# Kernel optimization log

Measured on AMD Instinct MI355X. Metric: run time of the kernel, lower is better.

The kernel has to match this reference:

```python
import jax, jax.numpy as jnp
import numpy as np

B, S, D = 4, 2048, 1024
H, DK, DV = 16, 64, 64


def setup_inputs() -> dict:
    key = jax.random.key(0)
    ks = jax.random.split(key, 12)
    scale = 1.0 / np.sqrt(D)
    queries = jax.random.normal(ks[0], (B, S, D), dtype=jnp.float32)
    keys_ = jax.random.normal(ks[1], (B, S, D), dtype=jnp.float32)
    values = jax.random.normal(ks[2], (B, S, D), dtype=jnp.float32)
    # binary additive mask (1 = masked out), broadcastable over batch and heads
    mask = jax.random.randint(ks[3], (1, 1, S, S), 0, 2).astype(jnp.float32)
    Wq = jax.random.normal(ks[4], (D, H * DK), dtype=jnp.float32) * scale
    bq = jnp.zeros((H * DK,), dtype=jnp.float32)
    Wk = jax.random.normal(ks[5], (D, H * DK), dtype=jnp.float32) * scale
    bk = jnp.zeros((H * DK,), dtype=jnp.float32)
    Wv = jax.random.normal(ks[6], (D, H * DV), dtype=jnp.float32) * scale
    bv = jnp.zeros((H * DV,), dtype=jnp.float32)
    Wo = jax.random.normal(ks[7], (H * DV, D), dtype=jnp.float32) * scale
    bo = jnp.zeros((D,), dtype=jnp.float32)
    return {"queries": queries, "keys": keys_, "values": values, "mask": mask,
            "Wq": Wq, "bq": bq, "Wk": Wk, "bk": bk, "Wv": Wv, "bv": bv,
            "Wo": Wo, "bo": bo}


def reference(queries, keys, values, mask, Wq, bq, Wk, bk, Wv, bv, Wo, bo):
    b = queries.shape[0]
    # projections + split heads: [B, S, H*Dh] -> [B, H, S, Dh]
    q = (queries @ Wq + bq).reshape(b, -1, H, DK).transpose(0, 2, 1, 3)
    k = (keys @ Wk + bk).reshape(b, -1, H, DK).transpose(0, 2, 1, 3)
    v = (values @ Wv + bv).reshape(b, -1, H, DV).transpose(0, 2, 1, 3)
    scores = jnp.einsum("bhqd,bhkd->bhqk", q, k) / jnp.sqrt(jnp.float32(DK))
    scores = scores + mask * (-1e9)
    attn = jax.nn.softmax(scores, axis=-1)
    ctx = jnp.einsum("bhqk,bhkd->bhqd", attn, v)  # [B, H, S, DV]
    ctx = ctx.transpose(0, 2, 1, 3).reshape(b, -1, H * DV)
    return ctx @ Wo + bo
```

## Files before the change

kernel.cpp:

```cpp
#include <hip/hip_runtime.h>
#include <cstdint>
#include <cstddef>

typedef __attribute__((ext_vector_type(8))) short bf16x8;
typedef __attribute__((ext_vector_type(4))) short bf16x4;
typedef __attribute__((ext_vector_type(4))) float f32x4;

__device__ __forceinline__ unsigned short f2bf(float f) {
    union { float f; unsigned int u; } v; v.f = f;
    unsigned int r = v.u + 0x7FFFu + ((v.u >> 16) & 1u);
    return (unsigned short)(r >> 16);
}
__device__ __forceinline__ unsigned int pk2(float a, float b) {
    return (unsigned int)f2bf(a) | ((unsigned int)f2bf(b) << 16);
}
__device__ __forceinline__ unsigned int pkfast(float a, float b) {
    unsigned int ua = __builtin_bit_cast(unsigned int, a) + 0x8000u;
    unsigned int ub = __builtin_bit_cast(unsigned int, b) + 0x8000u;
    return __builtin_amdgcn_perm(ub, ua, 0x07060302u);
}

typedef __attribute__((address_space(1))) void gvoid;
typedef __attribute__((address_space(3))) void svoid;
__device__ __forceinline__ void ld16_lds(const void* g, void* l) {
    __builtin_amdgcn_global_load_lds((gvoid*)g, (svoid*)l, 16, 0, 0);
}

#define LDT 72
#define QSCALE 0.1803368801111204f

__global__ __launch_bounds__(256)
void prep_weights(const float* __restrict__ W0, const float* __restrict__ W1,
                  const float* __restrict__ W2, const float* __restrict__ W3,
                  unsigned short* __restrict__ T0, unsigned short* __restrict__ T1,
                  unsigned short* __restrict__ T2, unsigned short* __restrict__ T3)
{
    __shared__ float t[32][33];
    const int z = blockIdx.z;
    const float* W = (z == 0) ? W0 : (z == 1) ? W1 : (z == 2) ? W2 : W3;
    unsigned short* Wt = (z == 0) ? T0 : (z == 1) ? T1 : (z == 2) ? T2 : T3;
    const int n0 = blockIdx.x * 32, k0 = blockIdx.y * 32;
    const int tx = threadIdx.x & 31, ty = threadIdx.x >> 5;
#pragma unroll
    for (int i = 0; i < 4; i++)
        t[ty + 8 * i][tx] = W[(size_t)(k0 + ty + 8 * i) * 1024 + n0 + tx];
    __syncthreads();
#pragma unroll
    for (int i = 0; i < 4; i++)
        Wt[(size_t)(n0 + ty + 8 * i) * 1024 + k0 + tx] = f2bf(t[tx][ty + 8 * i]);
}

__global__ __launch_bounds__(256)
void mask_pack(const float* __restrict__ m, unsigned long long* __restrict__ bits)
{
    const int wv = (blockIdx.x << 2) | (threadIdx.x >> 6);
    const int lane = threadIdx.x & 63;
    for (int i = 0; i < 64; i++) {
        const size_t word = (size_t)wv * 64 + i;
        const float v = m[word * 64 + lane];
        unsigned long long b = __ballot(v != 0.0f);
        if (lane == 0) bits[word] = b;
    }
}

template <int MODE>
__global__ __launch_bounds__(256, 2)
void gemm128(const float* __restrict__ A32, const unsigned short* __restrict__ A16,
             const unsigned short* __restrict__ Wt, const float* __restrict__ bias,
             unsigned short* __restrict__ ob, float* __restrict__ of)
{
    __shared__ __align__(16) unsigned short sm[2 * 128 * LDT];
    unsigned short* As = sm;
    unsigned short* Bs = sm + 128 * LDT;

    const int tid  = threadIdx.x;
    const int lane = tid & 63;
    const int wave = tid >> 6;
    const int quad = lane >> 4;
    const int l16  = lane & 15;
    const int wr   = wave >> 1;
    const int wc   = wave & 1;

    const int m0 = blockIdx.x * 128;
    const int n0 = blockIdx.y * 128;

    const int sr = tid >> 1;
    const int sh = (tid & 1) << 4;

    f32x4 acc[4][4];
#pragma unroll
    for (int i = 0; i < 4; i++)
#pragma unroll
        for (int j = 0; j < 4; j++) acc[i][j] = (f32x4){0.f, 0.f, 0.f, 0.f};

    for (int kk = 0; kk < 1024; kk += 32) {
        if (MODE < 3) {
            const float* g = A32 + (size_t)(m0 + sr) * 1024 + kk + sh;
            float4 a0 = *(const float4*)(g);
            float4 a1 = *(const float4*)(g + 4);
            float4 a2 = *(const float4*)(g + 8);
            float4 a3 = *(const float4*)(g + 12);
            uint4 p0, p1;
            p0.x = pk2(a0.x, a0.y); p0.y = pk2(a0.z, a0.w);
            p0.z = pk2(a1.x, a1.y); p0.w = pk2(a1.z, a1.w);
            p1.x = pk2(a2.x, a2.y); p1.y = pk2(a2.z, a2.w);
            p1.z = pk2(a3.x, a3.y); p1.w = pk2(a3.z, a3.w);
            *(uint4*)&As[sr * LDT + sh]     = p0;
            *(uint4*)&As[sr * LDT + sh + 8] = p1;
        } else {
            const uint4* g = (const uint4*)(A16 + (size_t)(m0 + sr) * 1024 + kk + sh);
            *(uint4*)&As[sr * LDT + sh]     = g[0];
            *(uint4*)&As[sr * LDT + sh + 8] = g[1];
        }
        {
            const uint4* g = (const uint4*)(Wt + (size_t)(n0 + sr) * 1024 + kk + sh);
            *(uint4*)&Bs[sr * LDT + sh]     = g[0];
            *(uint4*)&Bs[sr * LDT + sh + 8] = g[1];
        }
        __syncthreads();

        bf16x8 af[4], bfr[4];
#pragma unroll
        for (int mt = 0; mt < 4; mt++)
            af[mt] = *(const bf16x8*)&As[(wr * 64 + mt * 16 + l16) * LDT + quad * 8];
#pragma unroll
        for (int nt = 0; nt < 4; nt++)
            bfr[nt] = *(const bf16x8*)&Bs[(wc * 64 + nt * 16 + l16) * LDT + quad * 8];
#pragma unroll
        for (int mt = 0; mt < 4; mt++)
#pragma unroll
            for (int nt = 0; nt < 4; nt++)
                acc[mt][nt] = __builtin_amdgcn_mfma_f32_16x16x32_bf16(af[mt], bfr[nt], acc[mt][nt], 0, 0, 0);
        __syncthreads();
    }

    float bv[4];
#pragma unroll
    for (int nt = 0; nt < 4; nt++) bv[nt] = bias[n0 + wc * 64 + nt * 16 + l16];

    if (MODE == 3) {
#pragma unroll
        for (int mt = 0; mt < 4; mt++) {
            const int m = m0 + wr * 64 + mt * 16 + quad * 4;
#pragma unroll
            for (int nt = 0; nt < 4; nt++) {
                const int n = n0 + wc * 64 + nt * 16 + l16;
#pragma unroll
                for (int r = 0; r < 4; r++)
                    of[(size_t)(m + r) * 1024 + n] = acc[mt][nt][r] + bv[nt];
            }
        }
    } else if (MODE == 0 || MODE == 1) {
#pragma unroll
        for (int mt = 0; mt < 4; mt++) {
            const int m = m0 + wr * 64 + mt * 16 + quad * 4;
            const int b = m >> 11;
#pragma unroll
            for (int nt = 0; nt < 4; nt++) {
                const int n = n0 + wc * 64 + nt * 16 + l16;
                const int h = n >> 6, dk = n & 63;
#pragma unroll
                for (int r = 0; r < 4; r++) {
                    const int s = (m + r) & 2047;
                    float o = acc[mt][nt][r] + bv[nt];
                    if (MODE == 0) o *= QSCALE;
                    ob[((size_t)((b << 4) + h) * 2048 + s) * 64 + dk] = f2bf(o);
                }
            }
        }
    } else {
        unsigned short* T = sm + wave * (64 * LDT);
#pragma unroll
        for (int mt = 0; mt < 4; mt++)
#pragma unroll
            for (int nt = 0; nt < 4; nt++)
#pragma unroll
                for (int r = 0; r < 4; r++)
                    T[(nt * 16 + l16) * LDT + mt * 16 + quad * 4 + r] = f2bf(acc[mt][nt][r] + bv[nt]);
        __syncthreads();
#pragma unroll
        for (int i = 0; i < 8; i++) {
            const int nl = i * 8 + (lane >> 3);
            const int mc = lane & 7;
            uint4 v = *(const uint4*)&T[nl * LDT + mc * 8];
            const int n  = n0 + wc * 64 + nl;
            const int mg = m0 + wr * 64 + mc * 8;
            const int b = mg >> 11, s = mg & 2047;
            const int h = n >> 6, dv = n & 63;
            *(uint4*)&ob[((size_t)((b << 4) + h) * 64 + dv) * 2048 + s] = v;
        }
    }
}

__global__ __launch_bounds__(256, 4)
void attn_kernel(const unsigned short* __restrict__ q,
                 const unsigned short* __restrict__ k,
                 const unsigned short* __restrict__ vT,
                 const unsigned int* __restrict__ mbits,
                 unsigned short* __restrict__ ctx)
{
    __shared__ __align__(16) unsigned short Ks[2][64 * 64];
    __shared__ __align__(16) unsigned short Vs[2][64 * 64];

    const int tid = threadIdx.x, lane = tid & 63, wave = tid >> 6;
    const int quad = lane >> 4, l16 = lane & 15;
    const int sw = l16 & 7;
    const int bid = blockIdx.x;
    const int qblk = bid & 15, h = (bid >> 4) & 15, b = bid >> 8;

    const unsigned short* qb = q  + (size_t)(b * 16 + h) * 2048 * 64;
    const unsigned short* kb = k  + (size_t)(b * 16 + h) * 2048 * 64;
    const unsigned short* vb = vT + (size_t)(b * 16 + h) * 64 * 2048;

    const int c0 = tid, c1 = 256 + tid;
    const int r0 = c0 >> 3, gcc0 = (c0 & 7) ^ (r0 & 7);
    const int r1 = c1 >> 3, gcc1 = (c1 & 7) ^ (r1 & 7);

    int qrow[2];
    bf16x8 qf[2][2];
    f32x4 O0[4], O1[4];
    float l_i[2] = {0.f, 0.f};
#pragma unroll
    for (int g = 0; g < 2; g++) {
        qrow[g] = qblk * 128 + wave * 32 + g * 16 + l16;
        qf[g][0] = *(const bf16x8*)&qb[qrow[g] * 64 + quad * 8];
        qf[g][1] = *(const bf16x8*)&qb[qrow[g] * 64 + 32 + quad * 8];
    }
#pragma unroll
    for (int i = 0; i < 4; i++) { O0[i] = (f32x4){0.f,0.f,0.f,0.f}; O1[i] = (f32x4){0.f,0.f,0.f,0.f}; }
    const unsigned int* mrow0 = mbits + (size_t)qrow[0] * 64;
    const unsigned int* mrow1 = mbits + (size_t)qrow[1] * 64;

    {
        ld16_lds((const char*)kb + (size_t)r0 * 128 + gcc0 * 16, (char*)Ks[0] + c0 * 16);
        ld16_lds((const char*)kb + (size_t)r1 * 128 + gcc1 * 16, (char*)Ks[0] + c1 * 16);
        ld16_lds((const char*)vb + (size_t)r0 * 4096 + gcc0 * 16, (char*)Vs[0] + c0 * 16);
        ld16_lds((const char*)vb + (size_t)r1 * 4096 + gcc1 * 16, (char*)Vs[0] + c1 * 16);
    }
    uint2 mwc0 = *(const uint2*)&mrow0[0];
    uint2 mwc1 = *(const uint2*)&mrow1[0];

    for (int it = 0; it < 32; ++it) {
        const int kt = it << 6;
        const int cur = it & 1, nxt = cur ^ 1;
        __syncthreads();

        if (it < 31) {
            const char* kg = (const char*)kb + (size_t)(kt + 64) * 128;
            const char* vg = (const char*)vb + (size_t)(kt + 64) * 2;
            ld16_lds(kg + (size_t)r0 * 128 + gcc0 * 16, (char*)Ks[nxt] + c0 * 16);
            ld16_lds(kg + (size_t)r1 * 128 + gcc1 * 16, (char*)Ks[nxt] + c1 * 16);
            ld16_lds(vg + (size_t)r0 * 4096 + gcc0 * 16, (char*)Vs[nxt] + c0 * 16);
            ld16_lds(vg + (size_t)r1 * 4096 + gcc1 * 16, (char*)Vs[nxt] + c1 * 16);
        }
        const int mi = (it < 31) ? ((kt + 64) >> 5) : 0;
        uint2 mwn0 = *(const uint2*)&mrow0[mi];
        uint2 mwn1 = *(const uint2*)&mrow1[mi];

        const unsigned short* Kc = Ks[cur];
        const unsigned short* Vc = Vs[cur];

        f32x4 S0[4], S1[4];
#pragma unroll
        for (int mt = 0; mt < 4; mt++) {
            const unsigned short* kp = Kc + (mt * 16 + l16) * 64;
            bf16x8 ka0 = *(const bf16x8*)&kp[((quad    ) ^ sw) * 8];
            bf16x8 ka1 = *(const bf16x8*)&kp[((4 + quad) ^ sw) * 8];
            f32x4 z0 = (f32x4){0.f,0.f,0.f,0.f};
            f32x4 z1 = (f32x4){0.f,0.f,0.f,0.f};
            z0 = __builtin_amdgcn_mfma_f32_16x16x32_bf16(ka0, qf[0][0], z0, 0, 0, 0);
            S0[mt] = __builtin_amdgcn_mfma_f32_16x16x32_bf16(ka1, qf[0][1], z0, 0, 0, 0);
            z1 = __builtin_amdgcn_mfma_f32_16x16x32_bf16(ka0, qf[1][0], z1, 0, 0, 0);
            S1[mt] = __builtin_amdgcn_mfma_f32_16x16x32_bf16(ka1, qf[1][1], z1, 0, 0, 0);
        }
        float sum0 = 0.f, sum1 = 0.f;
        bf16x4 pf0[4], pf1[4];
#pragma unroll
        for (int mt = 0; mt < 4; mt++) {
            const unsigned int wm0 = ((mt & 2) ? mwc0.y : mwc0.x) >> (((mt & 1) << 4) + (quad << 2));
            const unsigned int wm1 = ((mt & 2) ? mwc1.y : mwc1.x) >> (((mt & 1) << 4) + (quad << 2));
#pragma unroll
            for (int r = 0; r < 4; r++) {
                float s0 = ((wm0 >> r) & 1u) ? -1e8f : S0[mt][r];
                float s1 = ((wm1 >> r) & 1u) ? -1e8f : S1[mt][r];
                s0 = __builtin_amdgcn_exp2f(s0);
                s1 = __builtin_amdgcn_exp2f(s1);
                S0[mt][r] = s0; sum0 += s0;
                S1[mt][r] = s1; sum1 += s1;
            }
            uint2 u0, u1;
            u0.x = pkfast(S0[mt][0], S0[mt][1]); u0.y = pkfast(S0[mt][2], S0[mt][3]);
            u1.x = pkfast(S1[mt][0], S1[mt][1]); u1.y = pkfast(S1[mt][2], S1[mt][3]);
            pf0[mt] = __builtin_bit_cast(bf16x4, u0);
            pf1[mt] = __builtin_bit_cast(bf16x4, u1);
        }
        sum0 += __shfl_xor(sum0, 16); sum0 += __shfl_xor(sum0, 32);
        sum1 += __shfl_xor(sum1, 16); sum1 += __shfl_xor(sum1, 32);
        l_i[0] += sum0; l_i[1] += sum1;

#pragma unroll
        for (int dvt = 0; dvt < 4; dvt++) {
            const unsigned short* vp = Vc + (dvt * 16 + l16) * 64;
#pragma unroll
            for (int mt = 0; mt < 4; mt++) {
                uint2 vv = *(const uint2*)&vp[((2 * mt + (quad >> 1)) ^ sw) * 8 + (quad & 1) * 4];
                bf16x4 va = __builtin_bit_cast(bf16x4, vv);
                O0[dvt] = __builtin_amdgcn_mfma_f32_16x16x16bf16_1k(va, pf0[mt], O0[dvt], 0, 0, 0);
                O1[dvt] = __builtin_amdgcn_mfma_f32_16x16x16bf16_1k(va, pf1[mt], O1[dvt], 0, 0, 0);
            }
        }
        mwc0 = mwn0; mwc1 = mwn1;
    }
#pragma unroll
    for (int g = 0; g < 2; g++) {
        const float rl = __builtin_amdgcn_rcpf(l_i[g]);
        const f32x4* O = g ? O1 : O0;
#pragma unroll
        for (int dvt = 0; dvt < 4; dvt++) {
            uint2 st;
            st.x = pk2(O[dvt][0] * rl, O[dvt][1] * rl);
            st.y = pk2(O[dvt][2] * rl, O[dvt][3] * rl);
            *(uint2*)&ctx[(size_t)(b * 2048 + qrow[g]) * 1024 + h * 64 + dvt * 16 + quad * 4] = st;
        }
    }
}

extern "C" void kernel_launch(void* const* d_in, const int* in_sizes, int n_in,
                              void* d_out, int out_size, void* d_ws, size_t ws_size,
                              hipStream_t stream)
{
    const float* Qin = (const float*)d_in[0];
    const float* Kin = (const float*)d_in[1];
    const float* Vin = (const float*)d_in[2];
    const float* Msk = (const float*)d_in[3];
    const float* Wq  = (const float*)d_in[4];
    const float* bq  = (const float*)d_in[5];
    const float* Wk  = (const float*)d_in[6];
    const float* bk  = (const float*)d_in[7];
    const float* Wv  = (const float*)d_in[8];
    const float* bv  = (const float*)d_in[9];
    const float* Wo  = (const float*)d_in[10];
    const float* bo  = (const float*)d_in[11];

    unsigned short* w = (unsigned short*)d_ws;
    unsigned short* wtq  = w;
    unsigned short* wtk  = w + (1u << 20);
    unsigned short* wtv  = w + 2u * (1u << 20);
    unsigned short* wto  = w + 3u * (1u << 20);
    unsigned short* qb   = w + 4u * (1u << 20);
    unsigned short* kb   = qb + (1u << 23);
    unsigned short* vTb  = kb + (1u << 23);
    unsigned short* ctxb = vTb + (1u << 23);
    unsigned long long* mb = (unsigned long long*)(ctxb + (1u << 23));

    prep_weights<<<dim3(32, 32, 4), 256, 0, stream>>>(Wq, Wk, Wv, Wo, wtq, wtk, wtv, wto);
    mask_pack<<<256, 256, 0, stream>>>(Msk, mb);
    gemm128<0><<<dim3(64, 8), 256, 0, stream>>>(Qin, nullptr, wtq, bq, qb, nullptr);
    gemm128<1><<<dim3(64, 8), 256, 0, stream>>>(Kin, nullptr, wtk, bk, kb, nullptr);
    gemm128<2><<<dim3(64, 8), 256, 0, stream>>>(Vin, nullptr, wtv, bv, vTb, nullptr);
    attn_kernel<<<1024, 256, 0, stream>>>(qb, kb, vTb, (const unsigned int*)mb, ctxb);
    gemm128<3><<<dim3(64, 8), 256, 0, stream>>>(nullptr, ctxb, wto, bo, nullptr, (float*)d_out);
}
```

Baseline: 453.1 us.

## Pre-convert inputs to bf16 and stage GEMM tiles via direct global-to-LDS loads

Adds a separate pass that converts the fp32 query, key and value inputs to bf16 once. The projection GEMMs then load bf16 tiles straight into LDS with global_load_lds instead of loading fp32 into registers, converting, and storing. This removes the repeated per-tile conversion and halves the bytes each of the 8 column blocks re-reads, at the cost of an extra full read and write pass over the inputs. The LDS tile padding is also dropped, which risks bank conflicts on fragment reads. Separately, the attention softmax denominator's cross-lane shuffle reduction moves out of the key loop to a single reduction at the end.

```diff
diff --git a/kernel.cpp b/kernel.cpp
--- a/kernel.cpp
+++ b/kernel.cpp
@@ -26,8 +26,24 @@
     __builtin_amdgcn_global_load_lds((gvoid*)g, (svoid*)l, 16, 0, 0);
 }
 
-#define LDT 72
 #define QSCALE 0.1803368801111204f
+
+__global__ __launch_bounds__(256)
+void cvt_bf16(const float* __restrict__ A, const float* __restrict__ B,
+              const float* __restrict__ C,
+              unsigned short* __restrict__ oa, unsigned short* __restrict__ ob,
+              unsigned short* __restrict__ oc)
+{
+    const float* src = (blockIdx.y == 0) ? A : (blockIdx.y == 1) ? B : C;
+    unsigned short* dst = (blockIdx.y == 0) ? oa : (blockIdx.y == 1) ? ob : oc;
+    const size_t i = ((size_t)blockIdx.x * 256 + threadIdx.x) * 8;
+    float4 a = *(const float4*)(src + i);
+    float4 b = *(const float4*)(src + i + 4);
+    uint4 p;
+    p.x = pk2(a.x, a.y); p.y = pk2(a.z, a.w);
+    p.z = pk2(b.x, b.y); p.w = pk2(b.z, b.w);
+    *(uint4*)(dst + i) = p;
+}
 
 __global__ __launch_bounds__(256)
 void prep_weights(const float* __restrict__ W0, const float* __restrict__ W1,
@@ -65,13 +81,13 @@
 
 template <int MODE>
 __global__ __launch_bounds__(256, 2)
-void gemm128(const float* __restrict__ A32, const unsigned short* __restrict__ A16,
+void gemm128(const unsigned short* __restrict__ A,
              const unsigned short* __restrict__ Wt, const float* __restrict__ bias,
              unsigned short* __restrict__ ob, float* __restrict__ of)
 {
-    __shared__ __align__(16) unsigned short sm[2 * 128 * LDT];
+    __shared__ __align__(16) unsigned short sm[(MODE == 2) ? 18432 : 8192];
     unsigned short* As = sm;
-    unsigned short* Bs = sm + 128 * LDT;
+    unsigned short* Bs = sm + 4096;
 
     const int tid  = threadIdx.x;
     const int lane = tid & 63;
@@ -84,8 +100,11 @@
     const int m0 = blockIdx.x * 128;
     const int n0 = blockIdx.y * 128;
 
-    const int sr = tid >> 1;
-    const int sh = (tid & 1) << 4;
+    const int sr0 = tid >> 2,        sc0 = (tid & 3) << 4;
+    const int sr1 = sr0 + 64,        sc1 = sc0;
+
+    const char* Ab = (const char*)A  + (size_t)m0 * 2048;
+    const char* Bb = (const char*)Wt + (size_t)n0 * 2048;
 
     f32x4 acc[4][4];
 #pragma unroll
@@ -94,38 +113,20 @@
         for (int j = 0; j < 4; j++) acc[i][j] = (f32x4){0.f, 0.f, 0.f, 0.f};
 
     for (int kk = 0; kk < 1024; kk += 32) {
-        if (MODE < 3) {
-            const float* g = A32 + (size_t)(m0 + sr) * 1024 + kk + sh;
-            float4 a0 = *(const float4*)(g);
-            float4 a1 = *(const float4*)(g + 4);
-            float4 a2 = *(const float4*)(g + 8);
-            float4 a3 = *(const float4*)(g + 12);
-            uint4 p0, p1;
-            p0.x = pk2(a0.x, a0.y); p0.y = pk2(a0.z, a0.w);
-            p0.z = pk2(a1.x, a1.y); p0.w = pk2(a1.z, a1.w);
-            p1.x = pk2(a2.x, a2.y); p1.y = pk2(a2.z, a2.w);
-            p1.z = pk2(a3.x, a3.y); p1.w = pk2(a3.z, a3.w);
-            *(uint4*)&As[sr * LDT + sh]     = p0;
-            *(uint4*)&As[sr * LDT + sh + 8] = p1;
-        } else {
-            const uint4* g = (const uint4*)(A16 + (size_t)(m0 + sr) * 1024 + kk + sh);
-            *(uint4*)&As[sr * LDT + sh]     = g[0];
-            *(uint4*)&As[sr * LDT + sh + 8] = g[1];
-        }
-        {
-            const uint4* g = (const uint4*)(Wt + (size_t)(n0 + sr) * 1024 + kk + sh);
-            *(uint4*)&Bs[sr * LDT + sh]     = g[0];
-            *(uint4*)&Bs[sr * LDT + sh + 8] = g[1];
-        }
+        const int kb2 = kk * 2;
+        ld16_lds(Ab + (size_t)sr0 * 2048 + kb2 + sc0, (char*)As + tid * 16);
+        ld16_lds(Ab + (size_t)sr1 * 2048 + kb2 + sc1, (char*)As + (256 + tid) * 16);
+        ld16_lds(Bb + (size_t)sr0 * 2048 + kb2 + sc0, (char*)Bs + tid * 16);
+        ld16_lds(Bb + (size_t)sr1 * 2048 + kb2 + sc1, (char*)Bs + (256 + tid) * 16);
         __syncthreads();
 
         bf16x8 af[4], bfr[4];
 #pragma unroll
         for (int mt = 0; mt < 4; mt++)
-            af[mt] = *(const bf16x8*)&As[(wr * 64 + mt * 16 + l16) * LDT + quad * 8];
+            af[mt] = *(const bf16x8*)&As[(wr * 64 + mt * 16 + l16) * 32 + quad * 8];
 #pragma unroll
         for (int nt = 0; nt < 4; nt++)
-            bfr[nt] = *(const bf16x8*)&Bs[(wc * 64 + nt * 16 + l16) * LDT + quad * 8];
+            bfr[nt] = *(const bf16x8*)&Bs[(wc * 64 + nt * 16 + l16) * 32 + quad * 8];
 #pragma unroll
         for (int mt = 0; mt < 4; mt++)
 #pragma unroll
@@ -169,20 +170,20 @@
             }
         }
     } else {
-        unsigned short* T = sm + wave * (64 * LDT);
+        unsigned short* T = sm + wave * (64 * 72);
 #pragma unroll
         for (int mt = 0; mt < 4; mt++)
 #pragma unroll
             for (int nt = 0; nt < 4; nt++)
 #pragma unroll
                 for (int r = 0; r < 4; r++)
-                    T[(nt * 16 + l16) * LDT + mt * 16 + quad * 4 + r] = f2bf(acc[mt][nt][r] + bv[nt]);
+                    T[(nt * 16 + l16) * 72 + mt * 16 + quad * 4 + r] = f2bf(acc[mt][nt][r] + bv[nt]);
         __syncthreads();
 #pragma unroll
         for (int i = 0; i < 8; i++) {
             const int nl = i * 8 + (lane >> 3);
             const int mc = lane & 7;
-            uint4 v = *(const uint4*)&T[nl * LDT + mc * 8];
+            uint4 v = *(const uint4*)&T[nl * 72 + mc * 8];
             const int n  = n0 + wc * 64 + nl;
             const int mg = m0 + wr * 64 + mc * 8;
             const int b = mg >> 11, s = mg & 2047;
@@ -294,8 +295,6 @@
             pf0[mt] = __builtin_bit_cast(bf16x4, u0);
             pf1[mt] = __builtin_bit_cast(bf16x4, u1);
         }
-        sum0 += __shfl_xor(sum0, 16); sum0 += __shfl_xor(sum0, 32);
-        sum1 += __shfl_xor(sum1, 16); sum1 += __shfl_xor(sum1, 32);
         l_i[0] += sum0; l_i[1] += sum1;
 
 #pragma unroll
@@ -313,7 +312,10 @@
     }
 #pragma unroll
     for (int g = 0; g < 2; g++) {
-        const float rl = __builtin_amdgcn_rcpf(l_i[g]);
+        float lsum = l_i[g];
+        lsum += __shfl_xor(lsum, 16);
+        lsum += __shfl_xor(lsum, 32);
+        const float rl = __builtin_amdgcn_rcpf(lsum);
         const f32x4* O = g ? O1 : O0;
 #pragma unroll
         for (int dvt = 0; dvt < 4; dvt++) {
@@ -347,17 +349,21 @@
     unsigned short* wtk  = w + (1u << 20);
     unsigned short* wtv  = w + 2u * (1u << 20);
     unsigned short* wto  = w + 3u * (1u << 20);
-    unsigned short* qb   = w + 4u * (1u << 20);
-    unsigned short* kb   = qb + (1u << 23);
-    unsigned short* vTb  = kb + (1u << 23);
-    unsigned short* ctxb = vTb + (1u << 23);
-    unsigned long long* mb = (unsigned long long*)(ctxb + (1u << 23));
+    unsigned short* qcv  = w + 4u * (1u << 20);
+    unsigned short* kcv  = qcv + (1u << 23);
+    unsigned short* vcv  = kcv + (1u << 23);
+    unsigned short* qb   = vcv + (1u << 23);
+    unsigned short* kb   = qb  + (1u << 23);
+    unsigned short* vTb  = kb  + (1u << 23);
+    unsigned short* ctxb = qcv;
+    unsigned long long* mb = (unsigned long long*)(vTb + (1u << 23));
 
     prep_weights<<<dim3(32, 32, 4), 256, 0, stream>>>(Wq, Wk, Wv, Wo, wtq, wtk, wtv, wto);
     mask_pack<<<256, 256, 0, stream>>>(Msk, mb);
-    gemm128<0><<<dim3(64, 8), 256, 0, stream>>>(Qin, nullptr, wtq, bq, qb, nullptr);
-    gemm128<1><<<dim3(64, 8), 256, 0, stream>>>(Kin, nullptr, wtk, bk, kb, nullptr);
-    gemm128<2><<<dim3(64, 8), 256, 0, stream>>>(Vin, nullptr, wtv, bv, vTb, nullptr);
+    cvt_bf16<<<dim3(4096, 3), 256, 0, stream>>>(Qin, Kin, Vin, qcv, kcv, vcv);
+    gemm128<0><<<dim3(64, 8), 256, 0, stream>>>(qcv, wtq, bq, qb, nullptr);
+    gemm128<1><<<dim3(64, 8), 256, 0, stream>>>(kcv, wtk, bk, kb, nullptr);
+    gemm128<2><<<dim3(64, 8), 256, 0, stream>>>(vcv, wtv, bv, vTb, nullptr);
     attn_kernel<<<1024, 256, 0, stream>>>(qb, kb, vTb, (const unsigned int*)mb, ctxb);
-    gemm128<3><<<dim3(64, 8), 256, 0, stream>>>(nullptr, ctxb, wto, bo, nullptr, (float*)d_out);
-}
+    gemm128<3><<<dim3(64, 8), 256, 0, stream>>>(ctxb, wto, bo, nullptr, (float*)d_out);
+}
```

Result: faster. 422.6 us (-6.7%).
